# Optimization experiments

Measured on AMD Instinct MI355X. Metric: run time of the kernel, lower is better.

The kernel has to match this reference:

```python
import jax, jax.numpy as jnp
import numpy as np

# Sizes: seq_len S, batch B, nodes N, embed D, candidates K, depth L (emb_depth=6)
S, B, N, D, K, L = 8, 16, 500, 128, 50, 6


def setup_inputs() -> dict:
    key = jax.random.key(0)
    ks = jax.random.split(key, 8)
    x = jax.random.uniform(ks[0], (S, B, N, 2), dtype=jnp.float32)  # TSP coords in [0,1)^2
    def w(k, shape, fan):
        return jax.random.normal(k, shape, dtype=jnp.float32) * (1.0 / np.sqrt(fan))
    Wn = w(ks[1], (2, D), 2)          # node (coord) encoder
    bn = jnp.zeros((D,), jnp.float32)
    Ws = w(ks[2], (L, D, D), D)       # per-layer self transform
    Wm = w(ks[3], (L, D, D), D)       # per-layer message transform
    bL = jnp.zeros((L, D), jnp.float32)
    we = jax.random.normal(ks[4], (L,), dtype=jnp.float32)  # per-layer edge-distance gate scale
    be = jnp.zeros((L,), jnp.float32)                        # per-layer edge-distance gate bias
    Wo = w(ks[5], (D, D), D)          # output projection after global mean pool
    return {"x": x, "Wn": Wn, "bn": bn, "Ws": Ws, "Wm": Wm, "bL": bL,
            "we": we, "be": be, "Wo": Wo}


def _forward(x, Wn, bn, Ws, Wm, bL, we, be, Wo):
    S_, B_, N_, F = x.shape
    G = S_ * B_
    coords = x.reshape(G, N_, F)                                  # (G,N,2)

    # --- candidate edge selection: per-node K nearest neighbors (cdist + top-k) ---
    diff = coords[:, :, None, :] - coords[:, None, :, :]          # (G,N,N,2)
    dist = jnp.sqrt(jnp.sum(diff * diff, axis=-1) + 1e-12)        # (G,N,N) euclidean cdist
    big = jnp.asarray(1e9, x.dtype)
    d_noself = dist + jnp.eye(N_, dtype=x.dtype) * big            # exclude self edges
    _, nn_idx = jax.lax.top_k(-d_noself, K)                       # (G,N,K) K smallest distances
    gi = jnp.arange(G)[:, None, None]
    ni = jnp.arange(N_)[None, :, None]
    A = jnp.zeros((G, N_, N_), x.dtype).at[gi, ni, nn_idx].set(1.0)
    A = jnp.maximum(A, jnp.swapaxes(A, 1, 2))                     # undirected, deduped edge set

    # --- GNN (Net: emb_depth=6 SiLU message-passing, distance-gated edges) ---
    h = jax.nn.silu(coords @ Wn + bn)                             # (G,N,D)
    for l in range(L):
        gate = jax.nn.silu(we[l] * dist + be[l]) * A              # (G,N,N) edge weights on kNN graph
        m = jnp.einsum('gij,gjd->gid', gate, h)                   # neighbor aggregation
        h = jax.nn.silu(h @ Ws[l] + m @ Wm[l] + bL[l])
    graph = jnp.mean(h, axis=1) @ Wo                              # global_mean_pool + proj (G,D)
    return graph.reshape(S_, B_, -1)                              # (S,B,D) node_embeddings


def reference(x, Wn, bn, Ws, Wm, bL, we, be, Wo):
    return _forward(x, Wn, bn, Ws, Wm, bL, we, be, Wo)
```

## Files before the change

kernel.cpp:

```cpp
#include <hip/hip_runtime.h>
#include <hip/hip_bf16.h>
#include <stdint.h>

#define G_   128
#define N_   500
#define NP_  512
#define D_   128
#define K_   50
#define L_   6
#define NW_  16
#define ROWT 125

typedef __attribute__((ext_vector_type(8))) short bf16x8;
typedef __attribute__((ext_vector_type(4))) float f32x4;

#define ADJ_BYTES  ((size_t)G_ * N_ * NW_ * 4)
#define EBUF_BYTES ((size_t)G_ * 32 * 1024 * 4)
#define ECNT_BYTES ((size_t)G_ * 32 * 4)
#define HB_BYTES   ((size_t)G_ * NP_ * D_ * 2)
#define WT_BYTES   ((size_t)L_ * D_ * D_ * 2)

#define L_B0   0
#define L_B1   32768
#define L_ECNT 69632
#define LDS_TOTAL 69664

__device__ __forceinline__ float silu_f(float z) {
    return z * __builtin_amdgcn_rcpf(1.0f + __expf(-z));
}
__device__ __forceinline__ unsigned short f2bf(float f) {
    uint32_t u = __float_as_uint(f);
    u += 0x7fffu + ((u >> 16) & 1u);
    return (unsigned short)(u >> 16);
}
__device__ __forceinline__ float bf2f(unsigned short s) {
    return __uint_as_float(((uint32_t)s) << 16);
}

__global__ __launch_bounds__(256) void knn_kernel(const float* __restrict__ x,
                                                  uint32_t* __restrict__ adj) {
    int g    = blockIdx.x / ROWT;
    int tile = blockIdx.x % ROWT;
    int wv   = threadIdx.x >> 6;
    int lane = threadIdx.x & 63;
    int i    = tile * 4 + wv;

    __shared__ float2 c[N_];
    for (int t = threadIdx.x; t < N_; t += 256)
        c[t] = ((const float2*)x)[(size_t)g * N_ + t];
    __syncthreads();

    float2 ci = c[i];
    uint32_t kb[8];
#pragma unroll
    for (int r = 0; r < 8; ++r) {
        int j = lane + r * 64;
        float dv;
        if (j < N_ && j != i) {
            float dx = ci.x - c[j].x, dy = ci.y - c[j].y;
            dv = dx * dx + dy * dy;
        } else {
            dv = 3.0e38f;
        }
        kb[r] = __float_as_uint(dv);
    }

    uint32_t prefix = 0;
    for (int bit = 28; bit >= 0; bit -= 2) {
        uint32_t c1 = prefix + (1u << bit);
        uint32_t c2 = prefix + (2u << bit);
        uint32_t c3 = prefix + (3u << bit);
        int n1 = 0, n2 = 0, n3 = 0;
#pragma unroll
        for (int r = 0; r < 8; ++r) {
            n1 += __popcll(__ballot(kb[r] < c1));
            n2 += __popcll(__ballot(kb[r] < c2));
            n3 += __popcll(__ballot(kb[r] < c3));
        }
        if (n3 < K_)      prefix = c3;
        else if (n2 < K_) prefix = c2;
        else if (n1 < K_) prefix = c1;
    }

    unsigned long long sel[8];
    int cntless = 0;
#pragma unroll
    for (int r = 0; r < 8; ++r) {
        sel[r] = __ballot(kb[r] < prefix);
        cntless += __popcll(sel[r]);
    }
    int rem = K_ - cntless;
    unsigned long long tb[8];
    int tietot = 0;
#pragma unroll
    for (int r = 0; r < 8; ++r) {
        tb[r] = __ballot(kb[r] == prefix);
        tietot += __popcll(tb[r]);
    }
    if (tietot == rem) {
#pragma unroll
        for (int r = 0; r < 8; ++r) sel[r] |= tb[r];
    } else {
#pragma unroll
        for (int r = 0; r < 8; ++r) {
            unsigned long long t2 = tb[r];
            while (rem > 0 && t2) {
                unsigned long long lb = t2 & (~t2 + 1ull);
                sel[r] |= lb;
                t2 ^= lb;
                --rem;
            }
        }
    }

    uint32_t* arow = adj + ((size_t)g * N_ + i) * NW_;
#pragma unroll
    for (int r = 0; r < 8; ++r) {
        if (lane == 2 * r)     arow[2 * r]     = (uint32_t)sel[r];
        if (lane == 2 * r + 1) arow[2 * r + 1] = (uint32_t)(sel[r] >> 32);
    }
}

__global__ __launch_bounds__(512) void ebuild_kernel(const float* __restrict__ x,
                                                     const uint32_t* __restrict__ adj,
                                                     uint32_t* __restrict__ ebuf,
                                                     uint32_t* __restrict__ ecnt) {
    int g = blockIdx.x, tid = threadIdx.x;
    __shared__ uint32_t am[N_][NW_];
    __shared__ float2   c[N_];
    __shared__ uint32_t bcnt[32];

    for (int t = tid; t < N_; t += 512)
        c[t] = ((const float2*)x)[(size_t)g * N_ + t];
    const uint32_t* ag = adj + (size_t)g * N_ * NW_;
    for (int t = tid; t < N_ * NW_; t += 512)
        ((uint32_t*)am)[t] = ag[t];
    if (tid < 32) bcnt[tid] = 0;
    __syncthreads();

    uint32_t buf[16];
    int cnt = 0;
    for (int idx = tid; idx < N_ * NW_; idx += 512) {
        int ii = idx >> 4, w = idx & 15;
        uint32_t v = am[ii][w];
        int jb = w << 5;
        int jmax = (jb + 32 <= N_) ? 32 : (N_ - jb);
        uint32_t wi = (uint32_t)ii >> 5, bi = ii & 31;
        for (int b = 0; b < jmax; ++b)
            v |= ((am[jb + b][wi] >> bi) & 1u) << b;
        buf[cnt++] = v;
    }
    __syncthreads();

    uint32_t* eg = ebuf + ((size_t)g << 15);
    cnt = 0;
    for (int idx = tid; idx < N_ * NW_; idx += 512) {
        int ii = idx >> 4, w = idx & 15;
        uint32_t v = buf[cnt++];
        if (!v) continue;
        float2 ci = c[ii];
        int il = ii & 127;
        int bb = (ii >> 7) << 3;
        while (v) {
            int b = __ffs(v) - 1;
            v &= v - 1;
            int j = (w << 5) + b;
            int bucket = bb + (j >> 6);
            uint32_t slot = atomicAdd(&bcnt[bucket], 1u);
            float dx = ci.x - c[j].x, dy = ci.y - c[j].y;
            float dd = sqrtf(dx * dx + dy * dy + 1e-12f);
            uint32_t rec = ((uint32_t)il << 25) | ((uint32_t)(j & 63) << 19)
                         | (__float_as_uint(dd) >> 11);
            if (slot < 1024u)
                eg[(bucket << 10) + slot] = rec;
        }
    }
    __syncthreads();
    if (tid < 32) ecnt[(g << 5) + tid] = bcnt[tid] > 1024u ? 1024u : bcnt[tid];
}

__global__ __launch_bounds__(256) void wprep_kernel(const float* __restrict__ Ws,
                                                    const float* __restrict__ Wm,
                                                    unsigned short* __restrict__ WsT,
                                                    unsigned short* __restrict__ WmT) {
    int idx = blockIdx.x * 256 + threadIdx.x;
    int half = idx >= L_ * D_ * D_;
    int r = half ? idx - L_ * D_ * D_ : idx;
    int l = r >> 14, rr = r & 16383, dout = rr >> 7, din = rr & 127;
    const float* W = half ? Wm : Ws;
    unsigned short* O = half ? WmT : WsT;
    O[r] = f2bf(W[(size_t)l * 16384 + din * 128 + dout]);
}

__global__ __launch_bounds__(256) void enc_kernel(const float* __restrict__ x,
                                                  const float* __restrict__ Wn,
                                                  const float* __restrict__ bn,
                                                  unsigned short* __restrict__ h,
                                                  unsigned short* __restrict__ hT) {
    int g = blockIdx.x, tid = threadIdx.x;
    __shared__ float2 c[N_];
    for (int t = tid; t < N_; t += 256)
        c[t] = ((const float2*)x)[(size_t)g * N_ + t];
    __syncthreads();
    for (int o = tid; o < N_ * 16; o += 256) {
        int i = o >> 4, d0 = (o & 15) * 8;
        float2 ci = c[i];
        unsigned short u[8];
#pragma unroll
        for (int e = 0; e < 8; ++e) {
            int d = d0 + e;
            u[e] = f2bf(silu_f(ci.x * Wn[d] + ci.y * Wn[D_ + d] + bn[d]));
        }
        *(uint4*)&h[((size_t)g * NP_ + i) * D_ + d0] = *(uint4*)u;
    }
    for (int o = tid; o < D_ * 64; o += 256) {
        int d = o >> 6, io = o & 63;
        float w0 = Wn[d], w1 = Wn[D_ + d], b = bn[d];
        unsigned short u[8];
#pragma unroll
        for (int e = 0; e < 8; ++e) {
            int i = io * 8 + e;
            unsigned short val = 0;
            if (i < N_) {
                float2 ci = c[i];
                val = f2bf(silu_f(ci.x * w0 + ci.y * w1 + b));
            }
            u[e] = val;
        }
        *(uint4*)&hT[((size_t)g * D_ + d) * NP_ + io * 8] = *(uint4*)u;
    }
}

__global__ __launch_bounds__(512, 4) void layer_kernel(
    const uint32_t* __restrict__ ebuf,
    const uint32_t* __restrict__ ecnt,
    const unsigned short* __restrict__ hin,
    const unsigned short* __restrict__ hinT,
    unsigned short* __restrict__ hout,
    unsigned short* __restrict__ houtT,
    const unsigned short* __restrict__ WsT,
    const unsigned short* __restrict__ WmT,
    const float* __restrict__ bL,
    const float* __restrict__ we,
    const float* __restrict__ be, int l)
{
    int bid = (blockIdx.x & 7) * 64 + (blockIdx.x >> 3);
    int g  = bid >> 2;
    int it = bid & 3;
    int i0 = it * 128;
    int tid = threadIdx.x;
    int lane = tid & 63, wv = tid >> 6;
    int wrow = wv >> 2, wcol = wv & 3;

    extern __shared__ char lds[];
    uint32_t* ecnt_s = (uint32_t*)(lds + L_ECNT);
    char* tileI = lds;
    char* tileT = lds + 34816;

    if (tid < 8) ecnt_s[tid] = ecnt[(g << 5) + (it << 3) + tid];

    float wel = we[l], bel = be[l];
    const unsigned short* hTg = hinT + (size_t)g * D_ * NP_;
    const uint32_t* ebg = ebuf + ((size_t)g << 15) + ((size_t)it << 13);

    auto zerogate = [&](char* buf) {
        char* gb = buf + 16384;
        const uint4 z4 = make_uint4(0u, 0u, 0u, 0u);
#pragma unroll
        for (int p = 0; p < 2; ++p)
            *(uint4*)(gb + (tid + p * 512) * 16) = z4;
    };
    auto stage = [&](char* buf, int jt) {
        char* hTA   = buf;
        char* gateB = buf + 16384;
        int j0t = jt * 64;
        uint4 hv[2];
#pragma unroll
        for (int p = 0; p < 2; ++p) {
            int o = tid + p * 512;
            int d = o >> 3, jo = o & 7;
            hv[p] = *(const uint4*)&hTg[(size_t)d * NP_ + j0t + jo * 8];
        }
        int n = (int)ecnt_s[jt];
        const uint32_t* eb = ebg + (jt << 10);
        for (int e = tid; e < n; e += 512) {
            uint32_t rec = eb[e];
            int il = rec >> 25;
            int jl = (rec >> 19) & 63;
            float dist = __uint_as_float((rec & 0x7FFFFu) << 11);
            float z = wel * dist + bel;
            float s = z * __builtin_amdgcn_rcpf(1.0f + __expf(-z));
            int byt = (il << 7) + (jl << 1);
            byt ^= (il & 7) << 4;
            *(unsigned short*)(gateB + byt) = f2bf(s);
        }
#pragma unroll
        for (int p = 0; p < 2; ++p) {
            int o = tid + p * 512;
            int d = o >> 3, jo = o & 7;
            int byt = (d << 7) + (jo << 4); byt ^= (d & 7) << 4;
            *(uint4*)(hTA + byt) = hv[p];
        }
    };

    f32x4 acc[4][2];
#pragma unroll
    for (int a_ = 0; a_ < 4; ++a_)
#pragma unroll
        for (int b_ = 0; b_ < 2; ++b_)
            acc[a_][b_] = (f32x4){0.f, 0.f, 0.f, 0.f};

    zerogate(lds + L_B0);
    zerogate(lds + L_B1);
    __syncthreads();
    stage(lds + L_B0, 0);
    __syncthreads();

    for (int jt = 0; jt < 8; ++jt) {
        char* cur = lds + ((jt & 1) ? L_B1 : L_B0);
        if (jt < 7) stage(lds + ((jt & 1) ? L_B0 : L_B1), jt + 1);
        char* hTA = cur, *gateB = cur + 16384;
#pragma unroll
        for (int kk = 0; kk < 64; kk += 32) {
            int kbyte = (kk + ((lane >> 4) << 3)) << 1;
            bf16x8 af[4], bfr[2];
#pragma unroll
            for (int fr = 0; fr < 4; ++fr) {
                int d = wrow * 64 + fr * 16 + (lane & 15);
                int byt = (d << 7) + kbyte; byt ^= (d & 7) << 4;
                af[fr] = *(const bf16x8*)(hTA + byt);
            }
#pragma unroll
            for (int fc = 0; fc < 2; ++fc) {
                int i = wcol * 32 + fc * 16 + (lane & 15);
                int byt = (i << 7) + kbyte; byt ^= (i & 7) << 4;
                bfr[fc] = *(const bf16x8*)(gateB + byt);
            }
#pragma unroll
            for (int fr = 0; fr < 4; ++fr)
#pragma unroll
                for (int fc = 0; fc < 2; ++fc)
                    acc[fr][fc] = __builtin_amdgcn_mfma_f32_16x16x32_bf16(
                        af[fr], bfr[fc], acc[fr][fc], 0, 0, 0);
        }
        __syncthreads();
        if (jt < 6) zerogate(cur);
        __syncthreads();
    }

    char* Bt = lds + L_B1;
    char* At = lds + L_B0;
#pragma unroll
    for (int fr = 0; fr < 4; ++fr)
#pragma unroll
        for (int fc = 0; fc < 2; ++fc) {
            int dbase = wrow * 64 + fr * 16 + ((lane >> 4) << 2);
            int ib    = wcol * 32 + fc * 16 + (lane & 15);
            f32x4 v = acc[fr][fc];
            uint32_t p0 = (uint32_t)f2bf(v[0]) | ((uint32_t)f2bf(v[1]) << 16);
            uint32_t p1 = (uint32_t)f2bf(v[2]) | ((uint32_t)f2bf(v[3]) << 16);
            int byt = (ib << 8) + (dbase << 1); byt ^= (ib & 7) << 4;
            *(uint32_t*)(Bt + byt)     = p0;
            *(uint32_t*)(Bt + byt + 4) = p1;
        }
    const unsigned short* wmp = WmT + (size_t)l * D_ * D_;
#pragma unroll
    for (int p = 0; p < 4; ++p) {
        int o = tid + p * 512;
        int dout = o >> 4, ko = o & 15;
        uint4 v = *(const uint4*)&wmp[dout * 128 + ko * 8];
        int byt = (dout << 8) + (ko << 4); byt ^= (dout & 7) << 4;
        *(uint4*)(At + byt) = v;
    }
    __syncthreads();

    f32x4 acc2[4][2];
#pragma unroll
    for (int a_ = 0; a_ < 4; ++a_)
#pragma unroll
        for (int b_ = 0; b_ < 2; ++b_)
            acc2[a_][b_] = (f32x4){0.f, 0.f, 0.f, 0.f};

    auto gemm128 = [&]() {
#pragma unroll
        for (int kk = 0; kk < 128; kk += 32) {
            int kbyte = (kk + ((lane >> 4) << 3)) << 1;
            bf16x8 af[4], bfr[2];
#pragma unroll
            for (int fr = 0; fr < 4; ++fr) {
                int d = wrow * 64 + fr * 16 + (lane & 15);
                int byt = (d << 8) + kbyte; byt ^= (d & 7) << 4;
                af[fr] = *(const bf16x8*)(At + byt);
            }
#pragma unroll
            for (int fc = 0; fc < 2; ++fc) {
                int i = wcol * 32 + fc * 16 + (lane & 15);
                int byt = (i << 8) + kbyte; byt ^= (i & 7) << 4;
                bfr[fc] = *(const bf16x8*)(Bt + byt);
            }
#pragma unroll
            for (int fr = 0; fr < 4; ++fr)
#pragma unroll
                for (int fc = 0; fc < 2; ++fc)
                    acc2[fr][fc] = __builtin_amdgcn_mfma_f32_16x16x32_bf16(
                        af[fr], bfr[fc], acc2[fr][fc], 0, 0, 0);
        }
    };
    gemm128();
    __syncthreads();

    const unsigned short* hg = hin + (size_t)g * NP_ * D_;
#pragma unroll
    for (int p = 0; p < 4; ++p) {
        int o = tid + p * 512;
        int il = o >> 4, ko = o & 15;
        int gi = i0 + il;
        uint4 v = make_uint4(0u, 0u, 0u, 0u);
        if (gi < N_) v = *(const uint4*)&hg[(size_t)gi * D_ + ko * 8];
        int byt = (il << 8) + (ko << 4); byt ^= (il & 7) << 4;
        *(uint4*)(Bt + byt) = v;
    }
    const unsigned short* wsp = WsT + (size_t)l * D_ * D_;
#pragma unroll
    for (int p = 0; p < 4; ++p) {
        int o = tid + p * 512;
        int dout = o >> 4, ko = o & 15;
        uint4 v = *(const uint4*)&wsp[dout * 128 + ko * 8];
        int byt = (dout << 8) + (ko << 4); byt ^= (dout & 7) << 4;
        *(uint4*)(At + byt) = v;
    }
    __syncthreads();
    gemm128();

    __syncthreads();
    const float* blp = bL + (size_t)l * D_;
#pragma unroll
    for (int fr = 0; fr < 4; ++fr)
#pragma unroll
        for (int fc = 0; fc < 2; ++fc) {
            int dbase = wrow * 64 + fr * 16 + ((lane >> 4) << 2);
            int ib = wcol * 32 + fc * 16 + (lane & 15);
            int gi = i0 + ib;
            f32x4 v = acc2[fr][fc];
            float4 bias = *(const float4*)&blp[dbase];
            float o0 = silu_f(v[0] + bias.x);
            float o1 = silu_f(v[1] + bias.y);
            float o2 = silu_f(v[2] + bias.z);
            float o3 = silu_f(v[3] + bias.w);
            if (gi >= N_) { o0 = 0.f; o1 = 0.f; o2 = 0.f; o3 = 0.f; }
            unsigned short b0 = f2bf(o0), b1 = f2bf(o1);
            unsigned short b2 = f2bf(o2), b3 = f2bf(o3);
            char* pI = tileI + ib * 272 + dbase * 2;
            *(uint32_t*)pI       = (uint32_t)b0 | ((uint32_t)b1 << 16);
            *(uint32_t*)(pI + 4) = (uint32_t)b2 | ((uint32_t)b3 << 16);
            *(unsigned short*)(tileT + (dbase    ) * 272 + ib * 2) = b0;
            *(unsigned short*)(tileT + (dbase + 1) * 272 + ib * 2) = b1;
            *(unsigned short*)(tileT + (dbase + 2) * 272 + ib * 2) = b2;
            *(unsigned short*)(tileT + (dbase + 3) * 272 + ib * 2) = b3;
        }
    __syncthreads();
    unsigned short* hgO  = hout  + (size_t)g * NP_ * D_;
    unsigned short* hgOT = houtT + (size_t)g * D_ * NP_;
#pragma unroll
    for (int p = 0; p < 4; ++p) {
        int o = tid + p * 512;
        int r = o >> 4, seg = o & 15;
        uint4 vI = *(const uint4*)(tileI + r * 272 + seg * 16);
        *(uint4*)&hgO[(size_t)(i0 + r) * D_ + seg * 8] = vI;
        uint4 vT = *(const uint4*)(tileT + r * 272 + seg * 16);
        *(uint4*)&hgOT[(size_t)r * NP_ + i0 + seg * 8] = vT;
    }
}

__global__ __launch_bounds__(256) void pool_kernel(const unsigned short* __restrict__ h,
                                                   const float* __restrict__ Wo,
                                                   float* __restrict__ out) {
    int g = blockIdx.x, tid = threadIdx.x;
    const unsigned short* hg = h + (size_t)g * NP_ * D_;
    float a8[8];
#pragma unroll
    for (int e = 0; e < 8; ++e) a8[e] = 0.f;
    int d0 = (tid & 15) * 8;
    for (int i = tid >> 4; i < N_; i += 16) {
        uint4 v = *(const uint4*)&hg[(size_t)i * D_ + d0];
        const unsigned short* pu = (const unsigned short*)&v;
#pragma unroll
        for (int e = 0; e < 8; ++e) a8[e] += bf2f(pu[e]);
    }
    __shared__ float red[16][D_];
#pragma unroll
    for (int e = 0; e < 8; ++e) red[tid >> 4][d0 + e] = a8[e];
    __syncthreads();
    __shared__ float pooled[D_];
    if (tid < D_) {
        float s = 0.f;
#pragma unroll
        for (int grp = 0; grp < 16; ++grp) s += red[grp][tid];
        pooled[tid] = s * (1.0f / (float)N_);
    }
    __syncthreads();
    if (tid < D_) {
        float accv = 0.f;
        for (int k = 0; k < D_; ++k) accv += pooled[k] * Wo[(size_t)k * D_ + tid];
        out[(size_t)g * D_ + tid] = accv;
    }
}

extern "C" void kernel_launch(void* const* d_in, const int* in_sizes, int n_in,
                              void* d_out, int out_size, void* d_ws, size_t ws_size,
                              hipStream_t stream) {
    (void)in_sizes; (void)n_in; (void)out_size; (void)ws_size;
    const float* x  = (const float*)d_in[0];
    const float* Wn = (const float*)d_in[1];
    const float* bn = (const float*)d_in[2];
    const float* Ws = (const float*)d_in[3];
    const float* Wm = (const float*)d_in[4];
    const float* bL = (const float*)d_in[5];
    const float* we = (const float*)d_in[6];
    const float* be = (const float*)d_in[7];
    const float* Wo = (const float*)d_in[8];
    float* out = (float*)d_out;

    char* w = (char*)d_ws;
    uint32_t*       adj  = (uint32_t*)w;        w += ADJ_BYTES;
    uint32_t*       ebuf = (uint32_t*)w;        w += EBUF_BYTES;
    uint32_t*       ecnt = (uint32_t*)w;        w += ECNT_BYTES;
    unsigned short* hA   = (unsigned short*)w;  w += HB_BYTES;
    unsigned short* hAT  = (unsigned short*)w;  w += HB_BYTES;
    unsigned short* hB   = (unsigned short*)w;  w += HB_BYTES;
    unsigned short* hBT  = (unsigned short*)w;  w += HB_BYTES;
    unsigned short* WsT  = (unsigned short*)w;  w += WT_BYTES;
    unsigned short* WmT  = (unsigned short*)w;  w += WT_BYTES;

    hipFuncSetAttribute((const void*)layer_kernel,
                        hipFuncAttributeMaxDynamicSharedMemorySize, LDS_TOTAL);

    knn_kernel<<<G_ * ROWT, 256, 0, stream>>>(x, adj);
    ebuild_kernel<<<G_, 512, 0, stream>>>(x, adj, ebuf, ecnt);
    wprep_kernel<<<(2 * L_ * D_ * D_) / 256, 256, 0, stream>>>(Ws, Wm, WsT, WmT);
    enc_kernel<<<G_, 256, 0, stream>>>(x, Wn, bn, hA, hAT);

    for (int l = 0; l < L_; ++l) {
        const unsigned short* hi  = (l & 1) ? hB  : hA;
        const unsigned short* hiT = (l & 1) ? hBT : hAT;
        unsigned short* ho  = (l & 1) ? hA  : hB;
        unsigned short* hoT = (l & 1) ? hAT : hBT;
        layer_kernel<<<G_ * 4, 512, LDS_TOTAL, stream>>>(ebuf, ecnt, hi, hiT, ho, hoT,
                                                         WsT, WmT, bL, we, be, l);
    }

    pool_kernel<<<G_, 256, 0, stream>>>(hA, Wo, out);
}
```

Before: 483.6 us.

## Prefetch next tile into registers during MFMA and simplify radix select

The layer kernel now loads the next tile's hT slice and edge records into registers before the current tile's MFMA loop, and writes them to LDS only after the barrier. This is meant to hide global-load latency behind compute instead of stalling at the start of each stage. The kNN threshold search changes from a 2-bit-per-step radix search with three ballots to a 1-bit-per-step search with a single ballot. The acc2 registers are also reused as acc to lower register pressure. In exchange the edge reads assume at most 1024 records per tile, and the loop unroll adds register pressure.

```diff
diff --git a/kernel.cpp b/kernel.cpp
--- a/kernel.cpp
+++ b/kernel.cpp
@@ -66,20 +66,13 @@
     }
 
     uint32_t prefix = 0;
-    for (int bit = 28; bit >= 0; bit -= 2) {
-        uint32_t c1 = prefix + (1u << bit);
-        uint32_t c2 = prefix + (2u << bit);
-        uint32_t c3 = prefix + (3u << bit);
-        int n1 = 0, n2 = 0, n3 = 0;
-#pragma unroll
-        for (int r = 0; r < 8; ++r) {
-            n1 += __popcll(__ballot(kb[r] < c1));
-            n2 += __popcll(__ballot(kb[r] < c2));
-            n3 += __popcll(__ballot(kb[r] < c3));
-        }
-        if (n3 < K_)      prefix = c3;
-        else if (n2 < K_) prefix = c2;
-        else if (n1 < K_) prefix = c1;
+    for (int bit = 29; bit >= 0; --bit) {
+        uint32_t cand = prefix | (1u << bit);
+        int cnt = 0;
+#pragma unroll
+        for (int r = 0; r < 8; ++r)
+            cnt += __popcll(__ballot(kb[r] < cand));
+        if (cnt < K_) prefix = cand;
     }
 
     unsigned long long sel[8];
@@ -263,43 +256,45 @@
     const unsigned short* hTg = hinT + (size_t)g * D_ * NP_;
     const uint32_t* ebg = ebuf + ((size_t)g << 15) + ((size_t)it << 13);
 
+    int d_st  = tid >> 3, jo_st = tid & 7;
+    size_t hoff0 = (size_t)d_st * NP_ + jo_st * 8;
+    size_t hoff1 = (size_t)(d_st + 64) * NP_ + jo_st * 8;
+    int hbyt0 = (d_st << 7) + (jo_st << 4); hbyt0 ^= (d_st & 7) << 4;
+    int hbyt1 = ((d_st + 64) << 7) + (jo_st << 4); hbyt1 ^= (d_st & 7) << 4;
+
     auto zerogate = [&](char* buf) {
         char* gb = buf + 16384;
         const uint4 z4 = make_uint4(0u, 0u, 0u, 0u);
-#pragma unroll
-        for (int p = 0; p < 2; ++p)
-            *(uint4*)(gb + (tid + p * 512) * 16) = z4;
+        *(uint4*)(gb + tid * 16)         = z4;
+        *(uint4*)(gb + (tid + 512) * 16) = z4;
     };
-    auto stage = [&](char* buf, int jt) {
-        char* hTA   = buf;
+    auto loadtile = [&](int jt, uint4* hv, uint32_t& ra, uint32_t& rb) {
+        int j0t = jt * 64;
+        hv[0] = *(const uint4*)&hTg[hoff0 + j0t];
+        hv[1] = *(const uint4*)&hTg[hoff1 + j0t];
+        const uint32_t* eb = ebg + (jt << 10);
+        ra = eb[tid];
+        rb = eb[tid + 512];
+    };
+    auto writetile = [&](char* buf, int jt, const uint4* hv, uint32_t ra, uint32_t rb) {
         char* gateB = buf + 16384;
-        int j0t = jt * 64;
-        uint4 hv[2];
-#pragma unroll
-        for (int p = 0; p < 2; ++p) {
-            int o = tid + p * 512;
-            int d = o >> 3, jo = o & 7;
-            hv[p] = *(const uint4*)&hTg[(size_t)d * NP_ + j0t + jo * 8];
-        }
+        *(uint4*)(buf + hbyt0) = hv[0];
+        *(uint4*)(buf + hbyt1) = hv[1];
         int n = (int)ecnt_s[jt];
-        const uint32_t* eb = ebg + (jt << 10);
-        for (int e = tid; e < n; e += 512) {
-            uint32_t rec = eb[e];
-            int il = rec >> 25;
-            int jl = (rec >> 19) & 63;
-            float dist = __uint_as_float((rec & 0x7FFFFu) << 11);
-            float z = wel * dist + bel;
-            float s = z * __builtin_amdgcn_rcpf(1.0f + __expf(-z));
-            int byt = (il << 7) + (jl << 1);
-            byt ^= (il & 7) << 4;
-            *(unsigned short*)(gateB + byt) = f2bf(s);
-        }
-#pragma unroll
-        for (int p = 0; p < 2; ++p) {
-            int o = tid + p * 512;
-            int d = o >> 3, jo = o & 7;
-            int byt = (d << 7) + (jo << 4); byt ^= (d & 7) << 4;
-            *(uint4*)(hTA + byt) = hv[p];
+#pragma unroll
+        for (int q = 0; q < 2; ++q) {
+            uint32_t rec = q ? rb : ra;
+            int e = tid + q * 512;
+            if (e < n) {
+                int il = rec >> 25;
+                int jl = (rec >> 19) & 63;
+                float dist = __uint_as_float((rec & 0x7FFFFu) << 11);
+                float z = wel * dist + bel;
+                float s = z * __builtin_amdgcn_rcpf(1.0f + __expf(-z));
+                int byt = (il << 7) + (jl << 1);
+                byt ^= (il & 7) << 4;
+                *(unsigned short*)(gateB + byt) = f2bf(s);
+            }
         }
     };
 
@@ -312,13 +307,20 @@
 
     zerogate(lds + L_B0);
     zerogate(lds + L_B1);
-    __syncthreads();
-    stage(lds + L_B0, 0);
-    __syncthreads();
-
+    {
+        uint4 hv0[2]; uint32_t ra0, rb0;
+        loadtile(0, hv0, ra0, rb0);
+        __syncthreads();
+        writetile(lds + L_B0, 0, hv0, ra0, rb0);
+    }
+    __syncthreads();
+
+#pragma unroll
     for (int jt = 0; jt < 8; ++jt) {
         char* cur = lds + ((jt & 1) ? L_B1 : L_B0);
-        if (jt < 7) stage(lds + ((jt & 1) ? L_B0 : L_B1), jt + 1);
+        char* nxt = lds + ((jt & 1) ? L_B0 : L_B1);
+        uint4 hvn[2]; uint32_t ra, rb;
+        if (jt < 7) loadtile(jt + 1, hvn, ra, rb);
         char* hTA = cur, *gateB = cur + 16384;
 #pragma unroll
         for (int kk = 0; kk < 64; kk += 32) {
@@ -345,6 +347,7 @@
         }
         __syncthreads();
         if (jt < 6) zerogate(cur);
+        if (jt < 7) writetile(nxt, jt + 1, hvn, ra, rb);
         __syncthreads();
     }
 
@@ -372,14 +375,12 @@
         int byt = (dout << 8) + (ko << 4); byt ^= (dout & 7) << 4;
         *(uint4*)(At + byt) = v;
     }
-    __syncthreads();
-
-    f32x4 acc2[4][2];
 #pragma unroll
     for (int a_ = 0; a_ < 4; ++a_)
 #pragma unroll
         for (int b_ = 0; b_ < 2; ++b_)
-            acc2[a_][b_] = (f32x4){0.f, 0.f, 0.f, 0.f};
+            acc[a_][b_] = (f32x4){0.f, 0.f, 0.f, 0.f};
+    __syncthreads();
 
     auto gemm128 = [&]() {
 #pragma unroll
@@ -402,8 +403,8 @@
             for (int fr = 0; fr < 4; ++fr)
 #pragma unroll
                 for (int fc = 0; fc < 2; ++fc)
-                    acc2[fr][fc] = __builtin_amdgcn_mfma_f32_16x16x32_bf16(
-                        af[fr], bfr[fc], acc2[fr][fc], 0, 0, 0);
+                    acc[fr][fc] = __builtin_amdgcn_mfma_f32_16x16x32_bf16(
+                        af[fr], bfr[fc], acc[fr][fc], 0, 0, 0);
         }
     };
     gemm128();
@@ -441,7 +442,7 @@
             int dbase = wrow * 64 + fr * 16 + ((lane >> 4) << 2);
             int ib = wcol * 32 + fc * 16 + (lane & 15);
             int gi = i0 + ib;
-            f32x4 v = acc2[fr][fc];
+            f32x4 v = acc[fr][fc];
             float4 bias = *(const float4*)&blp[dbase];
             float o0 = silu_f(v[0] + bias.x);
             float o1 = silu_f(v[1] + bias.y);
```

Measured after the change: 502.6 us. 3.9% more time.
